# Kernel tuning notes

Hardware: AMD Instinct MI355X
Metric: run time of the kernel (lower is better)

## Reference

```python
import jax, jax.numpy as jnp
import numpy as np

NUM_CLUSTERS = 32
EPS = 1e-12

def _l2norm(v, axis):
    return v / jnp.maximum(jnp.linalg.norm(v, axis=axis, keepdims=True), EPS)

def setup_inputs() -> dict:
    key = jax.random.key(0)
    k1, k2, k3 = jax.random.split(key, 3)
    B, M, D, K = 64, 512, 2048, NUM_CLUSTERS
    init_sc = 1.0 / np.sqrt(D)
    x = jax.random.normal(k1, (B, M, D), dtype=jnp.float32)
    W = init_sc * jax.random.normal(k2, (K, D), dtype=jnp.float32)
    centroids = init_sc * jax.random.normal(k3, (K, D), dtype=jnp.float32)
    return {"x": x, "W": W, "centroids": centroids}

def reference(x, W, centroids):
    # x: [B, M, D] frame features; W: [K, D]; centroids: [K, D]
    xn = _l2norm(x, axis=-1)                              # per-frame L2 normalize
    sa = jax.nn.softmax(jnp.einsum('bmd,kd->bmk', xn, W), axis=-1)  # [B, M, K]
    # vlad[b,k,d] = sum_m sa[b,m,k] * (xn[b,m,d] - centroids[k,d])
    #            = (sa^T @ xn)[b,k,d] - colsum(sa)[b,k] * centroids[k,d]
    agg = jnp.einsum('bmk,bmd->bkd', sa, xn)              # [B, K, D]
    vlad = agg - jnp.sum(sa, axis=1)[..., None] * centroids[None]
    vlad = _l2norm(vlad, axis=2)                          # intra-normalize per cluster
    vlad = vlad.reshape(vlad.shape[0], -1)                # [B, K*D]
    return _l2norm(vlad, axis=1)
```

## Files before the change

### kernel.cpp

```cpp
#include <hip/hip_runtime.h>
#include <hip/hip_bf16.h>
#include <cstdint>
#include <cstddef>

#define Bn 64
#define Mn 512
#define Dn 2048
#define Kn 32
#define EPSF 1e-12f

typedef __attribute__((ext_vector_type(8))) __bf16 bf16x8;
typedef __attribute__((ext_vector_type(4))) float f32x4;

__global__ __launch_bounds__(256) void k0_prep(const float* __restrict__ W,
                                               __bf16* __restrict__ Wb,
                                               float* __restrict__ colsum,
                                               float* __restrict__ ssq) {
  int idx = blockIdx.x * 256 + threadIdx.x;
  if (idx < Kn * Dn) Wb[idx] = (__bf16)W[idx];
  if (idx < Bn * Kn) { colsum[idx] = 0.f; ssq[idx] = 0.f; }
}

__global__ __launch_bounds__(256) void k1_logits_softmax(const float* __restrict__ x,
                                                         const __bf16* __restrict__ Wb,
                                                         __bf16* __restrict__ saP,
                                                         float* __restrict__ colsum) {
  int wv = threadIdx.x >> 6, lane = threadIdx.x & 63;
  int mr = lane & 15, q = lane >> 4;
  int row0 = (blockIdx.x * 4 + wv) * 16;
  int b = row0 >> 9;
  const float* xp = x + (size_t)(row0 + mr) * Dn + q * 8;
  const __bf16* wp = Wb + (size_t)mr * Dn + q * 8;
  f32x4 acc0 = {0.f, 0.f, 0.f, 0.f};
  f32x4 acc1 = {0.f, 0.f, 0.f, 0.f};
  float ssq = 0.f;
#pragma unroll 2
  for (int s = 0; s < 64; ++s) {
    f32x4 xa = *(const f32x4*)(xp + s * 32);
    f32x4 xb = *(const f32x4*)(xp + s * 32 + 4);
    bf16x8 af;
    af[0] = (__bf16)xa[0]; af[1] = (__bf16)xa[1];
    af[2] = (__bf16)xa[2]; af[3] = (__bf16)xa[3];
    af[4] = (__bf16)xb[0]; af[5] = (__bf16)xb[1];
    af[6] = (__bf16)xb[2]; af[7] = (__bf16)xb[3];
    ssq = fmaf(xa[0], xa[0], ssq); ssq = fmaf(xa[1], xa[1], ssq);
    ssq = fmaf(xa[2], xa[2], ssq); ssq = fmaf(xa[3], xa[3], ssq);
    ssq = fmaf(xb[0], xb[0], ssq); ssq = fmaf(xb[1], xb[1], ssq);
    ssq = fmaf(xb[2], xb[2], ssq); ssq = fmaf(xb[3], xb[3], ssq);
    bf16x8 b0 = *(const bf16x8*)(wp + s * 32);
    bf16x8 b1 = *(const bf16x8*)(wp + (size_t)16 * Dn + s * 32);
    acc0 = __builtin_amdgcn_mfma_f32_16x16x32_bf16(af, b0, acc0, 0, 0, 0);
    acc1 = __builtin_amdgcn_mfma_f32_16x16x32_bf16(af, b1, acc1, 0, 0, 0);
  }
  ssq += __shfl_xor(ssq, 16);
  ssq += __shfl_xor(ssq, 32);
  float invb = 1.f / fmaxf(sqrtf(ssq), EPSF);
  float cs0 = 0.f, cs1 = 0.f;
#pragma unroll
  for (int r = 0; r < 4; ++r) {
    float inv = __shfl(invb, q * 4 + r);
    float v0 = acc0[r] * inv, v1 = acc1[r] * inv;
    float mx = fmaxf(v0, v1);
    mx = fmaxf(mx, __shfl_xor(mx, 1));
    mx = fmaxf(mx, __shfl_xor(mx, 2));
    mx = fmaxf(mx, __shfl_xor(mx, 4));
    mx = fmaxf(mx, __shfl_xor(mx, 8));
    float e0 = __expf(v0 - mx), e1 = __expf(v1 - mx);
    float sm = e0 + e1;
    sm += __shfl_xor(sm, 1); sm += __shfl_xor(sm, 2);
    sm += __shfl_xor(sm, 4); sm += __shfl_xor(sm, 8);
    float rs = 1.f / sm;
    float sa0 = e0 * rs, sa1 = e1 * rs;
    size_t ro = (size_t)(row0 + q * 4 + r) * Kn;
    saP[ro + mr]      = (__bf16)(sa0 * inv);
    saP[ro + mr + 16] = (__bf16)(sa1 * inv);
    cs0 += sa0; cs1 += sa1;
  }
  cs0 += __shfl_xor(cs0, 16); cs0 += __shfl_xor(cs0, 32);
  cs1 += __shfl_xor(cs1, 16); cs1 += __shfl_xor(cs1, 32);
  if (lane < 16) {
    atomicAdd(&colsum[b * Kn + mr], cs0);
    atomicAdd(&colsum[b * Kn + mr + 16], cs1);
  }
}

#define MT 128
__global__ __launch_bounds__(256) void k3_agg(const float* __restrict__ x,
                                              const __bf16* __restrict__ saP,
                                              const float* __restrict__ colsum,
                                              const float* __restrict__ cent,
                                              float* __restrict__ vlad,
                                              float* __restrict__ ssq) {
  __shared__ float sa_t[MT * Kn];
  __shared__ float csl[Kn];
  int b = blockIdx.x >> 3;
  int d = (blockIdx.x & 7) * 256 + threadIdx.x;
  int t = threadIdx.x;
  if (t < Kn) csl[t] = colsum[b * Kn + t];
  float acc[Kn];
#pragma unroll
  for (int k = 0; k < Kn; ++k) acc[k] = 0.f;
  const float* xb = x + (size_t)b * Mn * Dn + d;
  const __bf16* sb = saP + (size_t)b * Mn * Kn;
  for (int mt = 0; mt < Mn; mt += MT) {
    __syncthreads();
#pragma unroll
    for (int i = 0; i < 2; ++i) {
      int u = t + 256 * i;
      bf16x8 v8 = *(const bf16x8*)(sb + (size_t)(mt)*Kn + (size_t)u * 8);
#pragma unroll
      for (int j = 0; j < 8; ++j) sa_t[u * 8 + j] = (float)v8[j];
    }
    __syncthreads();
    const float* xp = xb + (size_t)mt * Dn;
#pragma unroll 2
    for (int mm = 0; mm < MT; mm += 4) {
      float xv0 = xp[0];
      float xv1 = xp[Dn];
      float xv2 = xp[2 * Dn];
      float xv3 = xp[3 * Dn];
      xp += 4 * Dn;
      const f32x4* sr0 = (const f32x4*)&sa_t[(mm + 0) * Kn];
      const f32x4* sr1 = (const f32x4*)&sa_t[(mm + 1) * Kn];
      const f32x4* sr2 = (const f32x4*)&sa_t[(mm + 2) * Kn];
      const f32x4* sr3 = (const f32x4*)&sa_t[(mm + 3) * Kn];
#pragma unroll
      for (int g = 0; g < 8; ++g) {
        f32x4 s0 = sr0[g], s1 = sr1[g], s2 = sr2[g], s3 = sr3[g];
#pragma unroll
        for (int c = 0; c < 4; ++c) {
          int k = g * 4 + c;
          acc[k] = fmaf(s0[c], xv0, acc[k]);
          acc[k] = fmaf(s1[c], xv1, acc[k]);
          acc[k] = fmaf(s2[c], xv2, acc[k]);
          acc[k] = fmaf(s3[c], xv3, acc[k]);
        }
      }
    }
  }
  int lane = t & 63;
#pragma unroll
  for (int k = 0; k < Kn; ++k) {
    float vv = acc[k] - csl[k] * cent[(size_t)k * Dn + d];
    vlad[((size_t)(b * Kn + k)) * Dn + d] = vv;
    float sq = vv * vv;
    sq += __shfl_xor(sq, 1);  sq += __shfl_xor(sq, 2);
    sq += __shfl_xor(sq, 4);  sq += __shfl_xor(sq, 8);
    sq += __shfl_xor(sq, 16); sq += __shfl_xor(sq, 32);
    if (lane == 0) atomicAdd(&ssq[b * Kn + k], sq);
  }
}

__global__ __launch_bounds__(256) void k4_norm(float* __restrict__ out,
                                               const float* __restrict__ ssq) {
  __shared__ float rk[Kn];
  __shared__ float us[Kn];
  int b = blockIdx.x >> 4;
  int t = threadIdx.x;
  if (t < Kn) {
    float ss = ssq[b * Kn + t];
    float r = 1.f / fmaxf(sqrtf(ss), EPSF);
    rk[t] = r;
    us[t] = ss * r * r;
  }
  __syncthreads();
  float S = 0.f;
#pragma unroll
  for (int k = 0; k < Kn; ++k) S += us[k];
  float s = 1.f / fmaxf(sqrtf(S), EPSF);
  int chunk = blockIdx.x & 15;
  size_t base = (size_t)b * (Kn * Dn) + (size_t)chunk * 4096;
  f32x4* p = (f32x4*)(out + base);
#pragma unroll
  for (int i = 0; i < 4; ++i) {
    int idx = t + 256 * i;
    int k = (chunk * 4096 + idx * 4) >> 11;
    f32x4 v = p[idx];
    float sc = rk[k] * s;
    v[0] *= sc; v[1] *= sc; v[2] *= sc; v[3] *= sc;
    p[idx] = v;
  }
}

extern "C" void kernel_launch(void* const* d_in, const int* in_sizes, int n_in,
                              void* d_out, int out_size, void* d_ws, size_t ws_size,
                              hipStream_t stream) {
  const float* x = (const float*)d_in[0];
  const float* W = (const float*)d_in[1];
  const float* cent = (const float*)d_in[2];
  float* out = (float*)d_out;
  char* ws = (char*)d_ws;
  __bf16* Wb = (__bf16*)ws;
  float* colsum = (float*)(ws + 131072);
  float* ssqb = (float*)(ws + 131072 + 8192);
  __bf16* saP = (__bf16*)(ws + 131072 + 16384);
  hipLaunchKernelGGL(k0_prep, dim3(256), dim3(256), 0, stream, W, Wb, colsum, ssqb);
  hipLaunchKernelGGL(k1_logits_softmax, dim3(512), dim3(256), 0, stream, x, Wb, saP, colsum);
  hipLaunchKernelGGL(k3_agg, dim3(512), dim3(256), 0, stream, x, saP, colsum, cent, out, ssqb);
  hipLaunchKernelGGL(k4_norm, dim3(1024), dim3(256), 0, stream, out, ssqb);
}
```

Before: 498.4 us.

## Use bf16 MFMA for aggregation with transposed soft-assignment layout

```diff
diff --git a/kernel.cpp b/kernel.cpp
--- a/kernel.cpp
+++ b/kernel.cpp
@@ -10,6 +10,7 @@
 #define EPSF 1e-12f
 
 typedef __attribute__((ext_vector_type(8))) __bf16 bf16x8;
+typedef __attribute__((ext_vector_type(4))) __bf16 bf16x4;
 typedef __attribute__((ext_vector_type(4))) float f32x4;
 
 __global__ __launch_bounds__(256) void k0_prep(const float* __restrict__ W,
@@ -23,7 +24,7 @@
 
 __global__ __launch_bounds__(256) void k1_logits_softmax(const float* __restrict__ x,
                                                          const __bf16* __restrict__ Wb,
-                                                         __bf16* __restrict__ saP,
+                                                         __bf16* __restrict__ saT,
                                                          float* __restrict__ colsum) {
   int wv = threadIdx.x >> 6, lane = threadIdx.x & 63;
   int mr = lane & 15, q = lane >> 4;
@@ -56,6 +57,7 @@
   ssq += __shfl_xor(ssq, 32);
   float invb = 1.f / fmaxf(sqrtf(ssq), EPSF);
   float cs0 = 0.f, cs1 = 0.f;
+  bf16x4 v40, v41;
 #pragma unroll
   for (int r = 0; r < 4; ++r) {
     float inv = __shfl(invb, q * 4 + r);
@@ -71,11 +73,14 @@
     sm += __shfl_xor(sm, 4); sm += __shfl_xor(sm, 8);
     float rs = 1.f / sm;
     float sa0 = e0 * rs, sa1 = e1 * rs;
-    size_t ro = (size_t)(row0 + q * 4 + r) * Kn;
-    saP[ro + mr]      = (__bf16)(sa0 * inv);
-    saP[ro + mr + 16] = (__bf16)(sa1 * inv);
+    v40[r] = (__bf16)(sa0 * inv);
+    v41[r] = (__bf16)(sa1 * inv);
     cs0 += sa0; cs1 += sa1;
   }
+  int mloc = row0 & 511;
+  __bf16* st = saT + ((size_t)(b * Kn + mr)) * Mn + mloc + q * 4;
+  *(bf16x4*)st = v40;
+  *(bf16x4*)(st + (size_t)16 * Mn) = v41;
   cs0 += __shfl_xor(cs0, 16); cs0 += __shfl_xor(cs0, 32);
   cs1 += __shfl_xor(cs1, 16); cs1 += __shfl_xor(cs1, 32);
   if (lane < 16) {
@@ -84,70 +89,61 @@
   }
 }
 
-#define MT 128
+#define AS 520
 __global__ __launch_bounds__(256) void k3_agg(const float* __restrict__ x,
-                                              const __bf16* __restrict__ saP,
+                                              const __bf16* __restrict__ saT,
                                               const float* __restrict__ colsum,
                                               const float* __restrict__ cent,
                                               float* __restrict__ vlad,
                                               float* __restrict__ ssq) {
-  __shared__ float sa_t[MT * Kn];
+  __shared__ __bf16 sal[Kn * AS];
   __shared__ float csl[Kn];
-  int b = blockIdx.x >> 3;
-  int d = (blockIdx.x & 7) * 256 + threadIdx.x;
+  int b = blockIdx.x >> 4;
+  int dchunk = (blockIdx.x & 15) * 128;
   int t = threadIdx.x;
+  const __bf16* sg = saT + (size_t)b * Kn * Mn;
+#pragma unroll
+  for (int i = 0; i < 8; ++i) {
+    int u = t + 256 * i;
+    int kr = u >> 6, off = (u & 63) * 8;
+    *(bf16x8*)&sal[kr * AS + off] = *(const bf16x8*)(sg + (size_t)kr * Mn + off);
+  }
   if (t < Kn) csl[t] = colsum[b * Kn + t];
-  float acc[Kn];
+  __syncthreads();
+  int w = t >> 6, lane = t & 63;
+  int n = lane & 15, q = lane >> 4;
+  int d0 = dchunk + w * 32;
+  const float* xg = x + (size_t)b * Mn * Dn;
+  f32x4 acc[2][2] = {};
+  for (int m0 = 0; m0 < Mn; m0 += 32) {
+    bf16x8 a0 = *(const bf16x8*)&sal[n * AS + m0 + q * 8];
+    bf16x8 a1 = *(const bf16x8*)&sal[(n + 16) * AS + m0 + q * 8];
 #pragma unroll
-  for (int k = 0; k < Kn; ++k) acc[k] = 0.f;
-  const float* xb = x + (size_t)b * Mn * Dn + d;
-  const __bf16* sb = saP + (size_t)b * Mn * Kn;
-  for (int mt = 0; mt < Mn; mt += MT) {
-    __syncthreads();
+    for (int dt = 0; dt < 2; ++dt) {
+      const float* xp = xg + (size_t)(m0 + q * 8) * Dn + d0 + dt * 16 + n;
+      bf16x8 bv;
 #pragma unroll
-    for (int i = 0; i < 2; ++i) {
-      int u = t + 256 * i;
-      bf16x8 v8 = *(const bf16x8*)(sb + (size_t)(mt)*Kn + (size_t)u * 8);
+      for (int j = 0; j < 8; ++j) bv[j] = (__bf16)xp[(size_t)j * Dn];
+      acc[dt][0] = __builtin_amdgcn_mfma_f32_16x16x32_bf16(a0, bv, acc[dt][0], 0, 0, 0);
+      acc[dt][1] = __builtin_amdgcn_mfma_f32_16x16x32_bf16(a1, bv, acc[dt][1], 0, 0, 0);
+    }
+  }
 #pragma unroll
-      for (int j = 0; j < 8; ++j) sa_t[u * 8 + j] = (float)v8[j];
-    }
-    __syncthreads();
-    const float* xp = xb + (size_t)mt * Dn;
-#pragma unroll 2
-    for (int mm = 0; mm < MT; mm += 4) {
-      float xv0 = xp[0];
-      float xv1 = xp[Dn];
-      float xv2 = xp[2 * Dn];
-      float xv3 = xp[3 * Dn];
-      xp += 4 * Dn;
-      const f32x4* sr0 = (const f32x4*)&sa_t[(mm + 0) * Kn];
-      const f32x4* sr1 = (const f32x4*)&sa_t[(mm + 1) * Kn];
-      const f32x4* sr2 = (const f32x4*)&sa_t[(mm + 2) * Kn];
-      const f32x4* sr3 = (const f32x4*)&sa_t[(mm + 3) * Kn];
+  for (int dt = 0; dt < 2; ++dt) {
 #pragma unroll
-      for (int g = 0; g < 8; ++g) {
-        f32x4 s0 = sr0[g], s1 = sr1[g], s2 = sr2[g], s3 = sr3[g];
+    for (int kt = 0; kt < 2; ++kt) {
 #pragma unroll
-        for (int c = 0; c < 4; ++c) {
-          int k = g * 4 + c;
-          acc[k] = fmaf(s0[c], xv0, acc[k]);
-          acc[k] = fmaf(s1[c], xv1, acc[k]);
-          acc[k] = fmaf(s2[c], xv2, acc[k]);
-          acc[k] = fmaf(s3[c], xv3, acc[k]);
-        }
+      for (int r = 0; r < 4; ++r) {
+        int k = kt * 16 + q * 4 + r;
+        int d = d0 + dt * 16 + n;
+        float vv = acc[dt][kt][r] - csl[k] * cent[(size_t)k * Dn + d];
+        vlad[((size_t)(b * Kn + k)) * Dn + d] = vv;
+        float sq = vv * vv;
+        sq += __shfl_xor(sq, 1); sq += __shfl_xor(sq, 2);
+        sq += __shfl_xor(sq, 4); sq += __shfl_xor(sq, 8);
+        if (n == 0) atomicAdd(&ssq[b * Kn + k], sq);
       }
     }
-  }
-  int lane = t & 63;
-#pragma unroll
-  for (int k = 0; k < Kn; ++k) {
-    float vv = acc[k] - csl[k] * cent[(size_t)k * Dn + d];
-    vlad[((size_t)(b * Kn + k)) * Dn + d] = vv;
-    float sq = vv * vv;
-    sq += __shfl_xor(sq, 1);  sq += __shfl_xor(sq, 2);
-    sq += __shfl_xor(sq, 4);  sq += __shfl_xor(sq, 8);
-    sq += __shfl_xor(sq, 16); sq += __shfl_xor(sq, 32);
-    if (lane == 0) atomicAdd(&ssq[b * Kn + k], sq);
   }
 }
 
@@ -193,9 +189,9 @@
   __bf16* Wb = (__bf16*)ws;
   float* colsum = (float*)(ws + 131072);
   float* ssqb = (float*)(ws + 131072 + 8192);
-  __bf16* saP = (__bf16*)(ws + 131072 + 16384);
+  __bf16* saT = (__bf16*)(ws + 131072 + 16384);
   hipLaunchKernelGGL(k0_prep, dim3(256), dim3(256), 0, stream, W, Wb, colsum, ssqb);
-  hipLaunchKernelGGL(k1_logits_softmax, dim3(512), dim3(256), 0, stream, x, Wb, saP, colsum);
-  hipLaunchKernelGGL(k3_agg, dim3(512), dim3(256), 0, stream, x, saP, colsum, cent, out, ssqb);
+  hipLaunchKernelGGL(k1_logits_softmax, dim3(512), dim3(256), 0, stream, x, Wb, saT, colsum);
+  hipLaunchKernelGGL(k3_agg, dim3(1024), dim3(256), 0, stream, x, saT, colsum, cent, out, ssqb);
   hipLaunchKernelGGL(k4_norm, dim3(1024), dim3(256), 0, stream, out, ssqb);
 }
```

Result: faster. 447.8 us (-10.2%).
